# Kernel tuning notes

Measured on AMD Instinct MI355X. Metric: run time of the kernel, lower is better.

## Reference

```python
import jax, jax.numpy as jnp
import numpy as np

SEED_THR = 0.5
DUP_THR = 0.8


def _connected_labels(adj):
    """Min-label propagation with pointer jumping; adj: [N,N] bool (diag set for active nodes)."""
    N = adj.shape[0]

    def cond(carry):
        _, changed = carry
        return changed

    def body(carry):
        labels, _ = carry
        nbr_min = jnp.min(jnp.where(adj, labels[None, :], N), axis=1)
        new = jnp.minimum(labels, nbr_min)
        new = jnp.minimum(new, new[new])  # pointer jumping -> O(log N) convergence
        return new, jnp.any(new != labels)

    labels0 = jnp.arange(N)
    labels, _ = jax.lax.while_loop(cond, body, (labels0, jnp.array(True)))
    return labels


def _per_image(sig, scores):
    # sig: [N,C], scores: [N]
    N = sig.shape[0]
    idx = jnp.arange(N)
    sel = scores >= SEED_THR
    # fallback: if nothing passes the threshold, select argmax score
    sel = jnp.where(sel.any(), sel, idx == jnp.argmax(scores))

    # cosine pairwise similarity
    sn = sig * jax.lax.rsqrt(jnp.sum(sig * sig, axis=-1, keepdims=True) + 1e-12)
    sim = sn @ sn.T  # [N,N]

    adj = (sim >= DUP_THR) & sel[:, None] & sel[None, :]
    adj = adj | jnp.diag(sel)  # diagonal True for selected nodes

    labels = _connected_labels(adj)  # component root = min node index in component

    neg_inf = jnp.float32(-1e30)
    masked_scores = jnp.where(sel, scores, neg_inf)
    comp_max = jnp.full((N,), neg_inf, dtype=scores.dtype).at[labels].max(masked_scores)
    is_best = sel & (scores >= comp_max[labels])
    # tie-break: smallest index (matches torch argmax-first semantics)
    comp_best = jnp.full((N,), N, dtype=jnp.int32).at[labels].min(
        jnp.where(is_best, idx, N).astype(jnp.int32))
    is_seed = sel & (idx == comp_best[labels])

    # compact seeds to the front, ordered by component root (== DFS discovery order)
    sort_key = jnp.where(is_seed, labels, N)
    order = jnp.argsort(sort_key)
    mask = is_seed[order]  # [N] bool, True for valid seed slots
    seed_sig = jnp.where(mask[:, None], sig[order], jnp.zeros((), sig.dtype))
    seed_sc = jnp.where(mask, scores[order], jnp.zeros((), scores.dtype))
    return seed_sig, mask, seed_sc


def reference(query_signatures, query_seed_logits):
    L, B, Q, C = query_signatures.shape
    sig = jnp.transpose(query_signatures, (1, 0, 2, 3)).reshape(B, L * Q, C)
    logits = jnp.transpose(query_seed_logits, (1, 0, 2)).reshape(B, L * Q).astype(jnp.float32)
    scores = jax.nn.sigmoid(logits)
    seed_signatures, pad_mask, seed_scores = jax.vmap(_per_image)(sig, scores)
    return seed_signatures, pad_mask, seed_scores


def setup_inputs() -> dict:
    key = jax.random.key(0)
    k1, k2 = jax.random.split(key)
    L, B, Q, C = 6, 4, 900, 256
    return {
        "query_signatures": jax.random.normal(k1, (L, B, Q, C), dtype=jnp.float32),
        "query_seed_logits": jax.random.normal(k2, (L, B, Q), dtype=jnp.float32),
    }
```

## Files before the change

### kernel.cpp

```cpp
#include <hip/hip_runtime.h>
#include <cstdint>
#include <cstddef>

#define LDIM 6
#define BDIM 4
#define QDIM 900
#define CDIM 256
#define NDIM (LDIM*QDIM)
#define NN   5408
#define TT   85
#define NTRI (TT*(TT+1)/2)

typedef short bf16x8 __attribute__((ext_vector_type(8)));
typedef float floatx4 __attribute__((ext_vector_type(4)));

__device__ __forceinline__ int sig_off(int b, int n) {
    int l = n / QDIM, q = n - l * QDIM;
    return ((l * BDIM + b) * QDIM + q) * CDIM;
}
__device__ __forceinline__ int logit_off(int b, int n) {
    int l = n / QDIM, q = n - l * QDIM;
    return (l * BDIM + b) * QDIM + q;
}

__device__ __forceinline__ int uf_load(const int* p, int i) {
    return __hip_atomic_load(&p[i], __ATOMIC_RELAXED, __HIP_MEMORY_SCOPE_AGENT);
}
__device__ int uf_find(int* p, int x) {
    int r = x;
    int pr = uf_load(p, r);
    while (pr != r) { r = pr; pr = uf_load(p, r); }
    return r;
}
__device__ void uf_union(int* p, int a, int b) {
    int ra = uf_find(p, a), rb = uf_find(p, b);
    while (ra != rb) {
        int hi = ra > rb ? ra : rb;
        int lo = ra ^ rb ^ hi;
        int old = atomicCAS(&p[hi], hi, lo);
        if (old == hi) return;
        ra = uf_find(p, old);
        rb = uf_find(p, lo);
    }
}

__device__ __forceinline__ unsigned short f2bf(float f) {
    unsigned int u = __float_as_uint(f);
    u += 0x7fffu + ((u >> 16) & 1u);
    return (unsigned short)(u >> 16);
}

__global__ void k_init(const float* __restrict__ logits, float* __restrict__ scores,
                       int* __restrict__ sel, int* __restrict__ parent,
                       unsigned long long* __restrict__ argKey) {
    int b = blockIdx.y;
    int n = blockIdx.x * blockDim.x + threadIdx.x;
    unsigned long long key = 0ULL;
    if (n < NDIM) {
        float x = logits[logit_off(b, n)];
        float sc = 1.0f / (1.0f + expf(-x));
        scores[b * NN + n] = sc;
        sel[b * NN + n] = (sc >= 0.5f) ? 1 : 0;
        parent[b * NN + n] = n;
        key = ((unsigned long long)__float_as_uint(sc) << 32) | (unsigned int)(~n);
    }
    for (int off = 32; off; off >>= 1) {
        unsigned long long o = __shfl_down(key, off);
        if (o > key) key = o;
    }
    if ((threadIdx.x & 63) == 0) atomicMax(&argKey[b], key);
}

__global__ void k_compact(int* __restrict__ sel, int* __restrict__ selIdx,
                          int* __restrict__ Mcnt, const unsigned long long* __restrict__ argKey) {
    int b = blockIdx.x, t = threadIdx.x;
    int lane = t & 63, w = t >> 6;
    __shared__ int wsum[16];
    __shared__ int sbase;
    if (t == 0) sbase = 0;
    __syncthreads();
    for (int base = 0; base < NDIM; base += 1024) {
        int n = base + t;
        int f = (n < NDIM) ? sel[b * NN + n] : 0;
        unsigned long long bal = __ballot(f != 0);
        int rank = __popcll(bal & ((1ull << lane) - 1ull));
        if (lane == 0) wsum[w] = __popcll(bal);
        __syncthreads();
        if (t == 0) {
            int s = sbase;
            for (int i = 0; i < 16; i++) { int v = wsum[i]; wsum[i] = s; s += v; }
            sbase = s;
        }
        __syncthreads();
        if (f) selIdx[b * NN + wsum[w] + rank] = n;
        __syncthreads();
    }
    if (t == 0) {
        if (sbase == 0) {
            int n = (int)(~(unsigned int)(argKey[b] & 0xffffffffULL));
            selIdx[b * NN + 0] = n;
            sel[b * NN + n] = 1;
            Mcnt[b] = 1;
        } else {
            Mcnt[b] = sbase;
        }
    }
}

__global__ void k_tobf(const float* __restrict__ sig, const int* __restrict__ selIdx,
                       const int* __restrict__ Mcnt, unsigned short* __restrict__ Xbf) {
    int b = blockIdx.y;
    int g = (blockIdx.x * blockDim.x + threadIdx.x) >> 6;
    int lane = threadIdx.x & 63;
    if (g >= Mcnt[b]) return;
    int node = selIdx[b * NN + g];
    const float4 v = *(const float4*)(sig + sig_off(b, node) + lane * 4);
    float s = v.x * v.x + v.y * v.y + v.z * v.z + v.w * v.w;
    for (int off = 32; off; off >>= 1) s += __shfl_down(s, off);
    s = __shfl(s, 0);
    float ninv = rsqrtf(s + 1e-12f);
    ushort4 o;
    o.x = f2bf(v.x * ninv); o.y = f2bf(v.y * ninv);
    o.z = f2bf(v.z * ninv); o.w = f2bf(v.w * ninv);
    int c = lane >> 1;
    int sc = c ^ (g & 7);
    *(ushort4*)(Xbf + ((size_t)(b * NN + g)) * CDIM + sc * 8 + (lane & 1) * 4) = o;
}

__global__ __launch_bounds__(256) void k_sim_mfma(const unsigned short* __restrict__ Xbf,
                                                  const int* __restrict__ selIdx,
                                                  const int* __restrict__ Mcnt,
                                                  int* __restrict__ parent) {
    int bx = blockIdx.x;
    int b = bx & 3;
    int t = bx >> 2;
    int M = Mcnt[b];
    int ti = (int)((sqrtf(8.0f * (float)t + 1.0f) - 1.0f) * 0.5f);
    while ((ti + 1) * (ti + 2) / 2 <= t) ti++;
    while (ti * (ti + 1) / 2 > t) ti--;
    int tj = t - ti * (ti + 1) / 2;
    if (ti * 64 >= M) return;

    __shared__ char Bs[32768];

    int tid = threadIdx.x;
    int lane = tid & 63, wave = tid >> 6;
    int rsel = lane & 15, quad = lane >> 4;

    const char* xb = (const char*)Xbf + ((size_t)b * NN) * 512;
#pragma unroll
    for (int k = 0; k < 8; k++) {
        int i = wave * 8 + k;
        int row = min(tj * 64 + 2 * i, NN - 2);
        const char* src = xb + (size_t)row * 512 + lane * 16;
        __builtin_amdgcn_global_load_lds(
            (const __attribute__((address_space(1))) unsigned int*)src,
            (__attribute__((address_space(3))) unsigned int*)(Bs + i * 1024),
            16, 0, 0);
    }

    int gA = min(ti * 64 + wave * 16 + rsel, M - 1);
    const unsigned short* pA = Xbf + ((size_t)(b * NN + gA)) * CDIM;
    int swA = gA & 7;
    int swB = rsel & 7;

    __syncthreads();

    floatx4 acc[4] = {{0.f,0.f,0.f,0.f},{0.f,0.f,0.f,0.f},{0.f,0.f,0.f,0.f},{0.f,0.f,0.f,0.f}};
#pragma unroll
    for (int ks = 0; ks < CDIM / 32; ks++) {
        bf16x8 a = *(const bf16x8*)(pA + (((ks * 4 + quad) ^ swA) << 3));
#pragma unroll
        for (int nj = 0; nj < 4; nj++) {
            const char* pb = Bs + (nj * 16 + rsel) * 512 + (((ks * 4 + quad) ^ swB) << 4);
            bf16x8 bb = *(const bf16x8*)pb;
            acc[nj] = __builtin_amdgcn_mfma_f32_16x16x32_bf16(a, bb, acc[nj], 0, 0, 0);
        }
    }

    int rowA = ti * 64 + wave * 16 + quad * 4;
#pragma unroll
    for (int nj = 0; nj < 4; nj++) {
        int gj = tj * 64 + nj * 16 + rsel;
#pragma unroll
        for (int r = 0; r < 4; r++) {
            int gi = rowA + r;
            if (gi < M && gj < M && gi > gj && acc[nj][r] >= 0.8f) {
                uf_union(parent + b * NN, selIdx[b * NN + gi], selIdx[b * NN + gj]);
            }
        }
    }
}

__global__ void k_norm(const float* __restrict__ sig, float* __restrict__ ninv) {
    int b = blockIdx.y;
    int wave = (blockIdx.x * blockDim.x + threadIdx.x) >> 6;
    int lane = threadIdx.x & 63;
    if (wave >= NDIM) return;
    const float4 v = *(const float4*)(sig + sig_off(b, wave) + lane * 4);
    float s = v.x * v.x + v.y * v.y + v.z * v.z + v.w * v.w;
    for (int off = 32; off; off >>= 1) s += __shfl_down(s, off);
    if (lane == 0) ninv[b * NN + wave] = rsqrtf(s + 1e-12f);
}

__global__ __launch_bounds__(256) void k_sim(const float* __restrict__ sig,
                                             const float* __restrict__ ninv,
                                             const int* __restrict__ selIdx,
                                             const int* __restrict__ Mcnt,
                                             int* __restrict__ parent) {
    int b = blockIdx.y;
    int M = Mcnt[b];
    int t = blockIdx.x;
    int ti = (int)((sqrtf(8.0f * (float)t + 1.0f) - 1.0f) * 0.5f);
    while ((ti + 1) * (ti + 2) / 2 <= t) ti++;
    while (ti * (ti + 1) / 2 > t) ti--;
    int tj = t - ti * (ti + 1) / 2;
    if (ti * 64 >= M) return;

    __shared__ float As[64][17], Bs2[64][17];
    __shared__ int idxA[64], idxB[64], offA[64], offB[64];
    __shared__ float nvA[64], nvB[64];

    int tid = threadIdx.x;
    if (tid < 64) {
        int g = min(ti * 64 + tid, M - 1);
        int node = selIdx[b * NN + g];
        idxA[tid] = node; offA[tid] = sig_off(b, node); nvA[tid] = ninv[b * NN + node];
    } else if (tid < 128) {
        int lid = tid - 64;
        int g = min(tj * 64 + lid, M - 1);
        int node = selIdx[b * NN + g];
        idxB[lid] = node; offB[lid] = sig_off(b, node); nvB[lid] = ninv[b * NN + node];
    }
    __syncthreads();

    float acc[4][4] = {};
    int r = tid >> 2;
    int c4 = (tid & 3) * 4;
    int i0 = (tid >> 4) * 4;
    int j0 = (tid & 15) * 4;

    for (int k0 = 0; k0 < CDIM; k0 += 16) {
        float4 a = *(const float4*)(sig + offA[r] + k0 + c4);
        float4 bb = *(const float4*)(sig + offB[r] + k0 + c4);
        As[r][c4 + 0] = a.x; As[r][c4 + 1] = a.y; As[r][c4 + 2] = a.z; As[r][c4 + 3] = a.w;
        Bs2[r][c4 + 0] = bb.x; Bs2[r][c4 + 1] = bb.y; Bs2[r][c4 + 2] = bb.z; Bs2[r][c4 + 3] = bb.w;
        __syncthreads();
#pragma unroll
        for (int kk = 0; kk < 16; kk++) {
            float av[4], bv[4];
#pragma unroll
            for (int x = 0; x < 4; x++) { av[x] = As[i0 + x][kk]; bv[x] = Bs2[j0 + x][kk]; }
#pragma unroll
            for (int x = 0; x < 4; x++)
#pragma unroll
                for (int y = 0; y < 4; y++) acc[x][y] += av[x] * bv[y];
        }
        __syncthreads();
    }

#pragma unroll
    for (int x = 0; x < 4; x++)
#pragma unroll
        for (int y = 0; y < 4; y++) {
            int gi = ti * 64 + i0 + x, gj = tj * 64 + j0 + y;
            if (gi < M && gj < M && gi > gj) {
                float sim = acc[x][y] * nvA[i0 + x] * nvB[j0 + y];
                if (sim >= 0.8f) uf_union(parent + b * NN, idxA[i0 + x], idxB[j0 + y]);
            }
        }
}

__global__ void k_flatten(const int* __restrict__ parent, const int* __restrict__ sel,
                          const float* __restrict__ scores,
                          unsigned long long* __restrict__ compKey) {
    int b = blockIdx.y;
    int n = blockIdx.x * blockDim.x + threadIdx.x;
    if (n >= NDIM) return;
    if (!sel[b * NN + n]) return;
    int r = n, pr = parent[b * NN + r];
    while (pr != r) { r = pr; pr = parent[b * NN + r]; }
    unsigned long long key =
        ((unsigned long long)__float_as_uint(scores[b * NN + n]) << 32) | (unsigned int)(~n);
    atomicMax(&compKey[b * NN + r], key);
}

__global__ void k_rank(const unsigned long long* __restrict__ compKey,
                       int* __restrict__ seedNode, int* __restrict__ Scnt) {
    int b = blockIdx.x, t = threadIdx.x;
    int lane = t & 63, w = t >> 6;
    __shared__ int wsum[16];
    __shared__ int sbase;
    if (t == 0) sbase = 0;
    __syncthreads();
    for (int base = 0; base < NDIM; base += 1024) {
        int n = base + t;
        unsigned long long key = (n < NDIM) ? compKey[b * NN + n] : 0ULL;
        int f = (key != 0ULL) ? 1 : 0;
        unsigned long long bal = __ballot(f != 0);
        int rank = __popcll(bal & ((1ull << lane) - 1ull));
        if (lane == 0) wsum[w] = __popcll(bal);
        __syncthreads();
        if (t == 0) {
            int s = sbase;
            for (int i = 0; i < 16; i++) { int v = wsum[i]; wsum[i] = s; s += v; }
            sbase = s;
        }
        __syncthreads();
        if (f) seedNode[b * NN + wsum[w] + rank] = (int)(~(unsigned int)(key & 0xffffffffULL));
        __syncthreads();
    }
    if (t == 0) Scnt[b] = sbase;
}

__global__ void k_write(const float* __restrict__ sig, const float* __restrict__ scores,
                        const int* __restrict__ seedNode, const int* __restrict__ Scnt,
                        float* __restrict__ out) {
    int b = blockIdx.y;
    int slot = blockIdx.x;
    int lane = threadIdx.x;
    float* orow = out + ((size_t)(b * NDIM + slot)) * CDIM + lane * 4;
    if (slot < Scnt[b]) {
        int s = seedNode[b * NN + slot];
        float4 v = *(const float4*)(sig + sig_off(b, s) + lane * 4);
        *(float4*)orow = v;
        if (lane == 0) {
            out[(size_t)BDIM * NDIM * CDIM + (size_t)b * NDIM + slot] = 1.0f;
            out[(size_t)BDIM * NDIM * CDIM + (size_t)BDIM * NDIM + (size_t)b * NDIM + slot] =
                scores[b * NN + s];
        }
    } else {
        float4 z = {0.f, 0.f, 0.f, 0.f};
        *(float4*)orow = z;
        if (lane == 0) {
            out[(size_t)BDIM * NDIM * CDIM + (size_t)b * NDIM + slot] = 0.0f;
            out[(size_t)BDIM * NDIM * CDIM + (size_t)BDIM * NDIM + (size_t)b * NDIM + slot] = 0.0f;
        }
    }
}

extern "C" void kernel_launch(void* const* d_in, const int* in_sizes, int n_in,
                              void* d_out, int out_size, void* d_ws, size_t ws_size,
                              hipStream_t stream) {
    (void)in_sizes; (void)n_in; (void)out_size;
    const float* sig = (const float*)d_in[0];
    const float* logits = (const float*)d_in[1];
    float* out = (float*)d_out;
    char* ws = (char*)d_ws;

    const size_t arr = (size_t)BDIM * NN * 4;
    int* Mcnt = (int*)(ws + 16);
    int* Scnt = (int*)(ws + 32);
    unsigned long long* argKey = (unsigned long long*)(ws + 64);
    unsigned long long* compKey = (unsigned long long*)(ws + 256);
    float* scores = (float*)(ws + 256 + 2 * arr);
    int* sel      = (int*)(ws + 256 + 3 * arr);
    int* parent   = (int*)(ws + 256 + 4 * arr);
    int* selIdx   = (int*)(ws + 256 + 5 * arr);
    int* seedNode = (int*)(ws + 256 + 6 * arr);
    unsigned short* Xbf = (unsigned short*)(ws + 256 + 7 * arr);
    float* ninv   = (float*)(ws + 256 + 7 * arr);
    const size_t need_bf = 256 + 7 * arr + (size_t)BDIM * NN * CDIM * 2;

    hipMemsetAsync(d_ws, 0, 256 + 2 * arr, stream);

    dim3 gN((NDIM + 255) / 256, BDIM);
    k_init<<<gN, 256, 0, stream>>>(logits, scores, sel, parent, argKey);
    k_compact<<<BDIM, 1024, 0, stream>>>(sel, selIdx, Mcnt, argKey);

    if (ws_size >= need_bf) {
        k_tobf<<<dim3((NDIM + 3) / 4, BDIM), 256, 0, stream>>>(sig, selIdx, Mcnt, Xbf);
        k_sim_mfma<<<NTRI * BDIM, 256, 0, stream>>>(Xbf, selIdx, Mcnt, parent);
    } else {
        k_norm<<<dim3((NDIM + 3) / 4, BDIM), 256, 0, stream>>>(sig, ninv);
        k_sim<<<dim3(NTRI, BDIM), 256, 0, stream>>>(sig, ninv, selIdx, Mcnt, parent);
    }

    k_flatten<<<gN, 256, 0, stream>>>(parent, sel, scores, compKey);
    k_rank<<<BDIM, 1024, 0, stream>>>(compKey, seedNode, Scnt);
    k_write<<<dim3(NDIM, BDIM), 64, 0, stream>>>(sig, scores, seedNode, Scnt, out);
}
```

Measured before the change: 119.8 us.

## Fuse init/compact and flatten/rank kernels, drop memset and fp32 fallback

Merges the sigmoid/argmax init kernel into the compaction kernel, and the root-finding flatten kernel into the rank kernel. The combined rank kernel iterates only over selected nodes, and the per-block argmax reduction replaces the global atomicMax. The workspace memset is removed by zeroing compKey inside the fused kernel, the fp32 fallback path is dropped, and k_write now packs four rows per 256-thread block. Together these cut launch count and per-launch overhead, at the cost of doing init and flatten in only BDIM single blocks, which serialises that work.

New measurement: 115.7 us. 1.04x faster.

```diff
diff --git a/kernel.cpp b/kernel.cpp
--- a/kernel.cpp
+++ b/kernel.cpp
@@ -50,38 +50,32 @@
     return (unsigned short)(u >> 16);
 }
 
-__global__ void k_init(const float* __restrict__ logits, float* __restrict__ scores,
-                       int* __restrict__ sel, int* __restrict__ parent,
-                       unsigned long long* __restrict__ argKey) {
-    int b = blockIdx.y;
-    int n = blockIdx.x * blockDim.x + threadIdx.x;
-    unsigned long long key = 0ULL;
-    if (n < NDIM) {
-        float x = logits[logit_off(b, n)];
-        float sc = 1.0f / (1.0f + expf(-x));
-        scores[b * NN + n] = sc;
-        sel[b * NN + n] = (sc >= 0.5f) ? 1 : 0;
-        parent[b * NN + n] = n;
-        key = ((unsigned long long)__float_as_uint(sc) << 32) | (unsigned int)(~n);
-    }
-    for (int off = 32; off; off >>= 1) {
-        unsigned long long o = __shfl_down(key, off);
-        if (o > key) key = o;
-    }
-    if ((threadIdx.x & 63) == 0) atomicMax(&argKey[b], key);
-}
-
-__global__ void k_compact(int* __restrict__ sel, int* __restrict__ selIdx,
-                          int* __restrict__ Mcnt, const unsigned long long* __restrict__ argKey) {
+__global__ __launch_bounds__(1024) void k_prep(const float* __restrict__ logits,
+                                               float* __restrict__ scores,
+                                               int* __restrict__ parent,
+                                               int* __restrict__ selIdx,
+                                               int* __restrict__ Mcnt) {
     int b = blockIdx.x, t = threadIdx.x;
     int lane = t & 63, w = t >> 6;
     __shared__ int wsum[16];
+    __shared__ unsigned long long wkey[16];
     __shared__ int sbase;
     if (t == 0) sbase = 0;
+    unsigned long long mykey = 0ULL;
     __syncthreads();
     for (int base = 0; base < NDIM; base += 1024) {
         int n = base + t;
-        int f = (n < NDIM) ? sel[b * NN + n] : 0;
+        int f = 0;
+        if (n < NDIM) {
+            float x = logits[logit_off(b, n)];
+            float sc = 1.0f / (1.0f + expf(-x));
+            scores[b * NN + n] = sc;
+            parent[b * NN + n] = n;
+            f = (sc >= 0.5f) ? 1 : 0;
+            unsigned long long key =
+                ((unsigned long long)__float_as_uint(sc) << 32) | (unsigned int)(~n);
+            if (key > mykey) mykey = key;
+        }
         unsigned long long bal = __ballot(f != 0);
         int rank = __popcll(bal & ((1ull << lane) - 1ull));
         if (lane == 0) wsum[w] = __popcll(bal);
@@ -95,11 +89,17 @@
         if (f) selIdx[b * NN + wsum[w] + rank] = n;
         __syncthreads();
     }
+    for (int off = 32; off; off >>= 1) {
+        unsigned long long o = __shfl_down(mykey, off);
+        if (o > mykey) mykey = o;
+    }
+    if (lane == 0) wkey[w] = mykey;
+    __syncthreads();
     if (t == 0) {
         if (sbase == 0) {
-            int n = (int)(~(unsigned int)(argKey[b] & 0xffffffffULL));
-            selIdx[b * NN + 0] = n;
-            sel[b * NN + n] = 1;
+            unsigned long long k = 0ULL;
+            for (int i = 0; i < 16; i++) if (wkey[i] > k) k = wkey[i];
+            selIdx[b * NN + 0] = (int)(~(unsigned int)(k & 0xffffffffULL));
             Mcnt[b] = 1;
         } else {
             Mcnt[b] = sbase;
@@ -192,110 +192,42 @@
     }
 }
 
-__global__ void k_norm(const float* __restrict__ sig, float* __restrict__ ninv) {
-    int b = blockIdx.y;
-    int wave = (blockIdx.x * blockDim.x + threadIdx.x) >> 6;
-    int lane = threadIdx.x & 63;
-    if (wave >= NDIM) return;
-    const float4 v = *(const float4*)(sig + sig_off(b, wave) + lane * 4);
-    float s = v.x * v.x + v.y * v.y + v.z * v.z + v.w * v.w;
-    for (int off = 32; off; off >>= 1) s += __shfl_down(s, off);
-    if (lane == 0) ninv[b * NN + wave] = rsqrtf(s + 1e-12f);
-}
-
-__global__ __launch_bounds__(256) void k_sim(const float* __restrict__ sig,
-                                             const float* __restrict__ ninv,
-                                             const int* __restrict__ selIdx,
-                                             const int* __restrict__ Mcnt,
-                                             int* __restrict__ parent) {
-    int b = blockIdx.y;
-    int M = Mcnt[b];
-    int t = blockIdx.x;
-    int ti = (int)((sqrtf(8.0f * (float)t + 1.0f) - 1.0f) * 0.5f);
-    while ((ti + 1) * (ti + 2) / 2 <= t) ti++;
-    while (ti * (ti + 1) / 2 > t) ti--;
-    int tj = t - ti * (ti + 1) / 2;
-    if (ti * 64 >= M) return;
-
-    __shared__ float As[64][17], Bs2[64][17];
-    __shared__ int idxA[64], idxB[64], offA[64], offB[64];
-    __shared__ float nvA[64], nvB[64];
-
-    int tid = threadIdx.x;
-    if (tid < 64) {
-        int g = min(ti * 64 + tid, M - 1);
-        int node = selIdx[b * NN + g];
-        idxA[tid] = node; offA[tid] = sig_off(b, node); nvA[tid] = ninv[b * NN + node];
-    } else if (tid < 128) {
-        int lid = tid - 64;
-        int g = min(tj * 64 + lid, M - 1);
-        int node = selIdx[b * NN + g];
-        idxB[lid] = node; offB[lid] = sig_off(b, node); nvB[lid] = ninv[b * NN + node];
-    }
-    __syncthreads();
-
-    float acc[4][4] = {};
-    int r = tid >> 2;
-    int c4 = (tid & 3) * 4;
-    int i0 = (tid >> 4) * 4;
-    int j0 = (tid & 15) * 4;
-
-    for (int k0 = 0; k0 < CDIM; k0 += 16) {
-        float4 a = *(const float4*)(sig + offA[r] + k0 + c4);
-        float4 bb = *(const float4*)(sig + offB[r] + k0 + c4);
-        As[r][c4 + 0] = a.x; As[r][c4 + 1] = a.y; As[r][c4 + 2] = a.z; As[r][c4 + 3] = a.w;
-        Bs2[r][c4 + 0] = bb.x; Bs2[r][c4 + 1] = bb.y; Bs2[r][c4 + 2] = bb.z; Bs2[r][c4 + 3] = bb.w;
-        __syncthreads();
-#pragma unroll
-        for (int kk = 0; kk < 16; kk++) {
-            float av[4], bv[4];
-#pragma unroll
-            for (int x = 0; x < 4; x++) { av[x] = As[i0 + x][kk]; bv[x] = Bs2[j0 + x][kk]; }
-#pragma unroll
-            for (int x = 0; x < 4; x++)
-#pragma unroll
-                for (int y = 0; y < 4; y++) acc[x][y] += av[x] * bv[y];
-        }
-        __syncthreads();
-    }
-
-#pragma unroll
-    for (int x = 0; x < 4; x++)
-#pragma unroll
-        for (int y = 0; y < 4; y++) {
-            int gi = ti * 64 + i0 + x, gj = tj * 64 + j0 + y;
-            if (gi < M && gj < M && gi > gj) {
-                float sim = acc[x][y] * nvA[i0 + x] * nvB[j0 + y];
-                if (sim >= 0.8f) uf_union(parent + b * NN, idxA[i0 + x], idxB[j0 + y]);
-            }
-        }
-}
-
-__global__ void k_flatten(const int* __restrict__ parent, const int* __restrict__ sel,
-                          const float* __restrict__ scores,
-                          unsigned long long* __restrict__ compKey) {
-    int b = blockIdx.y;
-    int n = blockIdx.x * blockDim.x + threadIdx.x;
-    if (n >= NDIM) return;
-    if (!sel[b * NN + n]) return;
-    int r = n, pr = parent[b * NN + r];
-    while (pr != r) { r = pr; pr = parent[b * NN + r]; }
-    unsigned long long key =
-        ((unsigned long long)__float_as_uint(scores[b * NN + n]) << 32) | (unsigned int)(~n);
-    atomicMax(&compKey[b * NN + r], key);
-}
-
-__global__ void k_rank(const unsigned long long* __restrict__ compKey,
-                       int* __restrict__ seedNode, int* __restrict__ Scnt) {
+__global__ __launch_bounds__(1024) void k_comp(int* __restrict__ parent,
+                                               const int* __restrict__ selIdx,
+                                               const int* __restrict__ Mcnt,
+                                               const float* __restrict__ scores,
+                                               unsigned long long* __restrict__ compKey,
+                                               int* __restrict__ seedNode,
+                                               int* __restrict__ Scnt) {
     int b = blockIdx.x, t = threadIdx.x;
     int lane = t & 63, w = t >> 6;
     __shared__ int wsum[16];
     __shared__ int sbase;
+
+    for (int n = t; n < NN; n += 1024) compKey[b * NN + n] = 0ULL;
     if (t == 0) sbase = 0;
     __syncthreads();
+
+    int M = Mcnt[b];
+    for (int base = 0; base < M; base += 1024) {
+        int g = base + t;
+        if (g < M) {
+            int node = selIdx[b * NN + g];
+            int root = uf_find(parent + b * NN, node);
+            unsigned long long key =
+                ((unsigned long long)__float_as_uint(scores[b * NN + node]) << 32) |
+                (unsigned int)(~node);
+            atomicMax(&compKey[b * NN + root], key);
+        }
+    }
+    __syncthreads();
+
     for (int base = 0; base < NDIM; base += 1024) {
         int n = base + t;
-        unsigned long long key = (n < NDIM) ? compKey[b * NN + n] : 0ULL;
+        unsigned long long key = 0ULL;
+        if (n < NDIM)
+            key = __hip_atomic_load(&compKey[b * NN + n], __ATOMIC_RELAXED,
+                                    __HIP_MEMORY_SCOPE_AGENT);
         int f = (key != 0ULL) ? 1 : 0;
         unsigned long long bal = __ballot(f != 0);
         int rank = __popcll(bal & ((1ull << lane) - 1ull));
@@ -317,8 +249,8 @@
                         const int* __restrict__ seedNode, const int* __restrict__ Scnt,
                         float* __restrict__ out) {
     int b = blockIdx.y;
-    int slot = blockIdx.x;
-    int lane = threadIdx.x;
+    int slot = blockIdx.x * 4 + (threadIdx.x >> 6);
+    int lane = threadIdx.x & 63;
     float* orow = out + ((size_t)(b * NDIM + slot)) * CDIM + lane * 4;
     if (slot < Scnt[b]) {
         int s = seedNode[b * NN + slot];
@@ -342,41 +274,25 @@
 extern "C" void kernel_launch(void* const* d_in, const int* in_sizes, int n_in,
                               void* d_out, int out_size, void* d_ws, size_t ws_size,
                               hipStream_t stream) {
-    (void)in_sizes; (void)n_in; (void)out_size;
+    (void)in_sizes; (void)n_in; (void)out_size; (void)ws_size;
     const float* sig = (const float*)d_in[0];
     const float* logits = (const float*)d_in[1];
     float* out = (float*)d_out;
     char* ws = (char*)d_ws;
 
     const size_t arr = (size_t)BDIM * NN * 4;
-    int* Mcnt = (int*)(ws + 16);
-    int* Scnt = (int*)(ws + 32);
-    unsigned long long* argKey = (unsigned long long*)(ws + 64);
+    int* Mcnt = (int*)(ws + 0);
+    int* Scnt = (int*)(ws + 64);
     unsigned long long* compKey = (unsigned long long*)(ws + 256);
     float* scores = (float*)(ws + 256 + 2 * arr);
-    int* sel      = (int*)(ws + 256 + 3 * arr);
-    int* parent   = (int*)(ws + 256 + 4 * arr);
-    int* selIdx   = (int*)(ws + 256 + 5 * arr);
-    int* seedNode = (int*)(ws + 256 + 6 * arr);
-    unsigned short* Xbf = (unsigned short*)(ws + 256 + 7 * arr);
-    float* ninv   = (float*)(ws + 256 + 7 * arr);
-    const size_t need_bf = 256 + 7 * arr + (size_t)BDIM * NN * CDIM * 2;
-
-    hipMemsetAsync(d_ws, 0, 256 + 2 * arr, stream);
-
-    dim3 gN((NDIM + 255) / 256, BDIM);
-    k_init<<<gN, 256, 0, stream>>>(logits, scores, sel, parent, argKey);
-    k_compact<<<BDIM, 1024, 0, stream>>>(sel, selIdx, Mcnt, argKey);
-
-    if (ws_size >= need_bf) {
-        k_tobf<<<dim3((NDIM + 3) / 4, BDIM), 256, 0, stream>>>(sig, selIdx, Mcnt, Xbf);
-        k_sim_mfma<<<NTRI * BDIM, 256, 0, stream>>>(Xbf, selIdx, Mcnt, parent);
-    } else {
-        k_norm<<<dim3((NDIM + 3) / 4, BDIM), 256, 0, stream>>>(sig, ninv);
-        k_sim<<<dim3(NTRI, BDIM), 256, 0, stream>>>(sig, ninv, selIdx, Mcnt, parent);
-    }
-
-    k_flatten<<<gN, 256, 0, stream>>>(parent, sel, scores, compKey);
-    k_rank<<<BDIM, 1024, 0, stream>>>(compKey, seedNode, Scnt);
-    k_write<<<dim3(NDIM, BDIM), 64, 0, stream>>>(sig, scores, seedNode, Scnt, out);
-}
+    int* parent   = (int*)(ws + 256 + 3 * arr);
+    int* selIdx   = (int*)(ws + 256 + 4 * arr);
+    int* seedNode = (int*)(ws + 256 + 5 * arr);
+    unsigned short* Xbf = (unsigned short*)(ws + 256 + 6 * arr);
+
+    k_prep<<<BDIM, 1024, 0, stream>>>(logits, scores, parent, selIdx, Mcnt);
+    k_tobf<<<dim3((NDIM + 3) / 4, BDIM), 256, 0, stream>>>(sig, selIdx, Mcnt, Xbf);
+    k_sim_mfma<<<NTRI * BDIM, 256, 0, stream>>>(Xbf, selIdx, Mcnt, parent);
+    k_comp<<<BDIM, 1024, 0, stream>>>(parent, selIdx, Mcnt, scores, compKey, seedNode, Scnt);
+    k_write<<<dim3(NDIM / 4, BDIM), 256, 0, stream>>>(sig, scores, seedNode, Scnt, out);
+}
```
